# Optimization experiments

Measured on AMD Instinct MI355X. Metric: run time of the kernel, lower is better.

## Reference

```python
import jax, jax.numpy as jnp
import numpy as np
import math

B, LQ, LK = 2, 2048, 2048
DIM = 1024
H = 16
DH = DIM // H


def setup_inputs() -> dict:
    key = jax.random.key(0)
    ks = jax.random.split(key, 12)
    s = 1.0 / math.sqrt(DIM)
    return {
        "query": jax.random.normal(ks[0], (B, LQ, DIM), jnp.float32),
        "key": jax.random.normal(ks[1], (B, LK, DIM), jnp.float32),
        "value": jax.random.normal(ks[2], (B, LK, DIM), jnp.float32),
        "mask": jnp.zeros((B, LQ, LK), dtype=bool),
        "Wq": jax.random.normal(ks[3], (DIM, DIM), jnp.float32) * s,
        "bq": jax.random.normal(ks[4], (DIM,), jnp.float32) * s,
        "Wk": jax.random.normal(ks[5], (DIM, DIM), jnp.float32) * s,
        "bk": jax.random.normal(ks[6], (DIM,), jnp.float32) * s,
        "Wv": jax.random.normal(ks[7], (DIM, DIM), jnp.float32) * s,
        "bv": jax.random.normal(ks[8], (DIM,), jnp.float32) * s,
        "Wo": jax.random.normal(ks[9], (DIM, DIM), jnp.float32) * s,
        "bo": jax.random.normal(ks[10], (DIM,), jnp.float32) * s,
    }


def reference(query, key, value, mask, Wq, bq, Wk, bk, Wv, bv, Wo, bo):
    b = query.shape[0]

    def shape(x):  # (b, l, dim) -> (b, h, l, dh)
        return x.reshape(b, -1, H, DH).transpose(0, 2, 1, 3)

    q = shape(query @ Wq.T + bq)
    k = shape(key @ Wk.T + bk)
    v = shape(value @ Wv.T + bv)

    q = q / math.sqrt(DH)
    # (b, h, lq, lk) score matrix, computed in float32 as the original does
    scores = jnp.einsum("bhqd,bhkd->bhqk", q, k).astype(jnp.float32)
    scores = jnp.where(mask[:, None, :, :], jnp.float32(-1e18), scores)
    attn = jax.nn.softmax(scores, axis=-1).astype(q.dtype)
    context = jnp.einsum("bhqk,bhkd->bhqd", attn, v)
    context = context.transpose(0, 2, 1, 3).reshape(b, -1, H * DH)
    return context @ Wo.T + bo
```

## Files before the change

### kernel.cpp

```cpp
#include <hip/hip_runtime.h>
#include <hip/hip_bf16.h>

typedef __attribute__((ext_vector_type(4))) float float4v;
typedef __attribute__((ext_vector_type(8))) __bf16 bf16x8;
typedef __attribute__((ext_vector_type(4))) unsigned short ushort4v;
typedef __attribute__((ext_vector_type(8))) unsigned short ushort8v;

#define MFMA16(a, b, c) __builtin_amdgcn_mfma_f32_16x16x32_bf16(a, b, c, 0, 0, 0)

__device__ __forceinline__ unsigned short f2bf(float f) {
    return __builtin_bit_cast(unsigned short, (__bf16)f);
}

__device__ __forceinline__ float fast_exp2(float x) {
#if __has_builtin(__builtin_amdgcn_exp2f)
    return __builtin_amdgcn_exp2f(x);
#else
    return exp2f(x);
#endif
}

__device__ __forceinline__ void gl_lds16(const unsigned short* g, unsigned short* l) {
    __builtin_amdgcn_global_load_lds(
        (const __attribute__((address_space(1))) void*)g,
        (__attribute__((address_space(3))) void*)l, 16, 0, 0);
}

struct CvtSeg { const float* s; unsigned short* d; int n; };
struct Cvt4 { CvtSeg seg[4]; };

__global__ __launch_bounds__(256) void cvt_kernel(Cvt4 a) {
    const CvtSeg c = a.seg[blockIdx.y];
    const int stride = gridDim.x * 256 * 8;
    for (int i = (blockIdx.x * 256 + threadIdx.x) * 8; i < c.n; i += stride) {
        float4v v0 = *(const float4v*)(c.s + i);
        float4v v1 = *(const float4v*)(c.s + i + 4);
        ushort8v u;
        u[0] = f2bf(v0.x); u[1] = f2bf(v0.y); u[2] = f2bf(v0.z); u[3] = f2bf(v0.w);
        u[4] = f2bf(v1.x); u[5] = f2bf(v1.y); u[6] = f2bf(v1.z); u[7] = f2bf(v1.w);
        *(ushort8v*)(c.d + i) = u;
    }
}

__global__ __launch_bounds__(256) void gemm_qkv_kernel(
    const float* qa, const float* ka, const float* va,
    const unsigned short* Wqb, const unsigned short* Wkb, const unsigned short* Wvb,
    const float* bq, const float* bk, const float* bv,
    unsigned short* Qb, unsigned short* Kb, unsigned short* Vb, float qscale) {
    __shared__ unsigned short As[128 * 64];
    __shared__ unsigned short Ws[128 * 64];
    const int id = blockIdx.x;
    const int work = (id & 7) * 96 + (id >> 3);
    const int x = work & 31;
    const int combo = work >> 5;
    const int y = combo & 7;
    const int z = combo >> 3;
    const float* A = z == 0 ? qa : (z == 1 ? ka : va);
    const unsigned short* W = z == 0 ? Wqb : (z == 1 ? Wkb : Wvb);
    const float* bias = z == 0 ? bq : (z == 1 ? bk : bv);
    unsigned short* Cout = z == 0 ? Qb : (z == 1 ? Kb : Vb);
    const float scale = z == 0 ? qscale : 1.0f;
    const int m0 = x * 128, n0 = y * 128;
    const int N = 1024, K = 1024;

    const int t = threadIdx.x;
    const int w = t >> 6, lane = t & 63;
    const int quad = lane >> 4, l16 = lane & 15;
    const int wm = (w >> 1) * 64, wn = (w & 1) * 64;

    float4v acc[4][4];
    for (int i = 0; i < 4; ++i)
        for (int j = 0; j < 4; ++j) acc[i][j] = float4v{0.f, 0.f, 0.f, 0.f};

    const int srow = lane >> 3;
    const int scol = (lane & 7) * 8;

    for (int k0 = 0; k0 < K; k0 += 64) {
        float4v fa[4][2];
        for (int i = 0; i < 4; ++i) {
            const int c = w * 4 + i;
            const float* src = A + (size_t)(m0 + c * 8 + srow) * K + k0 + scol;
            fa[i][0] = *(const float4v*)src;
            fa[i][1] = *(const float4v*)(src + 4);
        }
        __syncthreads();
        for (int i = 0; i < 4; ++i) {
            const int c = w * 4 + i;
            ushort8v u;
            u[0] = f2bf(fa[i][0].x); u[1] = f2bf(fa[i][0].y);
            u[2] = f2bf(fa[i][0].z); u[3] = f2bf(fa[i][0].w);
            u[4] = f2bf(fa[i][1].x); u[5] = f2bf(fa[i][1].y);
            u[6] = f2bf(fa[i][1].z); u[7] = f2bf(fa[i][1].w);
            *(ushort8v*)&As[c * 512 + lane * 8] = u;
            gl_lds16(W + (size_t)(n0 + c * 8 + srow) * K + k0 + scol,
                     &Ws[c * 512 + lane * 8]);
        }
        __syncthreads();
        for (int ks = 0; ks < 2; ++ks) {
            bf16x8 af[4], wf[4];
            for (int i = 0; i < 4; ++i)
                af[i] = *(const bf16x8*)&As[(wm + i * 16 + l16) * 64 + ks * 32 + quad * 8];
            for (int i = 0; i < 4; ++i)
                wf[i] = *(const bf16x8*)&Ws[(wn + i * 16 + l16) * 64 + ks * 32 + quad * 8];
            for (int mi = 0; mi < 4; ++mi)
                for (int ni = 0; ni < 4; ++ni)
                    acc[mi][ni] = MFMA16(af[mi], wf[ni], acc[mi][ni]);
        }
    }

    for (int mi = 0; mi < 4; ++mi)
        for (int ni = 0; ni < 4; ++ni) {
            const int col = n0 + wn + ni * 16 + l16;
            const float bv = bias[col];
            for (int reg = 0; reg < 4; ++reg) {
                const int row = m0 + wm + mi * 16 + quad * 4 + reg;
                Cout[(size_t)row * N + col] = f2bf((acc[mi][ni][reg] + bv) * scale);
            }
        }
}

__global__ __launch_bounds__(256) void gemm_out_kernel(const unsigned short* __restrict__ A,
                                                       const unsigned short* __restrict__ W,
                                                       const float* __restrict__ bias,
                                                       float* __restrict__ Cout) {
    __shared__ unsigned short As[64 * 64];
    __shared__ unsigned short Ws[128 * 64];
    const int N = 1024, K = 1024;
    const int t = threadIdx.x;
    const int w = t >> 6, lane = t & 63;
    const int quad = lane >> 4, l16 = lane & 15;
    const int m0 = blockIdx.x * 64, n0 = blockIdx.y * 128;
    const int wm = (w & 1) * 32, wn = (w >> 1) * 64;

    float4v acc[2][4];
    for (int i = 0; i < 2; ++i)
        for (int j = 0; j < 4; ++j) acc[i][j] = float4v{0.f, 0.f, 0.f, 0.f};

    const int srow = lane >> 3;
    const int scol = (lane & 7) * 8;

    for (int k0 = 0; k0 < K; k0 += 64) {
        __syncthreads();
        for (int i = 0; i < 2; ++i) {
            const int c = w * 2 + i;
            gl_lds16(A + (size_t)(m0 + c * 8 + srow) * K + k0 + scol,
                     &As[c * 512 + lane * 8]);
        }
        for (int i = 0; i < 4; ++i) {
            const int c = w * 4 + i;
            gl_lds16(W + (size_t)(n0 + c * 8 + srow) * K + k0 + scol,
                     &Ws[c * 512 + lane * 8]);
        }
        __syncthreads();
        for (int ks = 0; ks < 2; ++ks) {
            bf16x8 af[2], wf[4];
            for (int i = 0; i < 2; ++i)
                af[i] = *(const bf16x8*)&As[(wm + i * 16 + l16) * 64 + ks * 32 + quad * 8];
            for (int i = 0; i < 4; ++i)
                wf[i] = *(const bf16x8*)&Ws[(wn + i * 16 + l16) * 64 + ks * 32 + quad * 8];
            for (int mi = 0; mi < 2; ++mi)
                for (int ni = 0; ni < 4; ++ni)
                    acc[mi][ni] = MFMA16(af[mi], wf[ni], acc[mi][ni]);
        }
    }

    for (int mi = 0; mi < 2; ++mi)
        for (int ni = 0; ni < 4; ++ni) {
            const int col = n0 + wn + ni * 16 + l16;
            const float bv = bias[col];
            for (int reg = 0; reg < 4; ++reg) {
                const int row = m0 + wm + mi * 16 + quad * 4 + reg;
                Cout[(size_t)row * N + col] = acc[mi][ni][reg] + bv;
            }
        }
}

__global__ __launch_bounds__(256) void attn_kernel(const unsigned short* __restrict__ Q,
                                                   const unsigned short* __restrict__ Kg,
                                                   const unsigned short* __restrict__ Vg,
                                                   const unsigned char* __restrict__ mask,
                                                   unsigned short* __restrict__ Ctx) {
    const int bid = blockIdx.x;
    const int bh = bid & 31;
    const int qt = bid >> 5;
    const int b = bh >> 4, h = bh & 15;
    const int t = threadIdx.x, w = t >> 6, lane = t & 63;
    const int quad = lane >> 4, l16 = lane & 15;

    __shared__ unsigned short Pt[128][72];
    __shared__ unsigned short Ks[64][72];
    __shared__ unsigned short Vt[64][72];

    const unsigned short* Qp = Q + ((size_t)(b * 2048 + qt * 128)) * 1024 + h * 64;
    const unsigned short* Kp = Kg + ((size_t)b * 2048) * 1024 + h * 64;
    const unsigned short* Vp = Vg + ((size_t)b * 2048) * 1024 + h * 64;
    const unsigned char* Mp = mask + (size_t)(b * 2048 + qt * 128) * 2048;

    for (int p = 0; p < 4; ++p) {
        const int idx = t + p * 256;
        const int r = idx >> 3, c8 = (idx & 7) * 8;
        *(uint4*)&Pt[r][c8] = *(const uint4*)(Qp + (size_t)r * 1024 + c8);
    }
    __syncthreads();
    bf16x8 qf[2][2];
    for (int c = 0; c < 2; ++c)
        for (int ks = 0; ks < 2; ++ks)
            qf[c][ks] = *(const bf16x8*)&Pt[w * 32 + c * 16 + l16][ks * 32 + quad * 8];

    float4v o[2][4];
    for (int c = 0; c < 2; ++c)
        for (int i = 0; i < 4; ++i) o[c][i] = float4v{0.f, 0.f, 0.f, 0.f};
    float l_acc[2] = {0.f, 0.f};

    const int sr = t >> 3, sc8 = (t & 7) * 8;
    const int vkk = (t & 31) * 2, vd0 = (t >> 5) * 8;
    const int mrow = w * 32 + (lane >> 1);
    const int mc0 = (lane & 1) * 32;

    uint4 kreg0, kreg1, vreg0, vreg1, mreg0, mreg1;
    {
        kreg0 = *(const uint4*)(Kp + (size_t)sr * 1024 + sc8);
        kreg1 = *(const uint4*)(Kp + (size_t)(sr + 32) * 1024 + sc8);
        vreg0 = *(const uint4*)(Vp + (size_t)vkk * 1024 + vd0);
        vreg1 = *(const uint4*)(Vp + (size_t)(vkk + 1) * 1024 + vd0);
        mreg0 = *(const uint4*)(Mp + (size_t)mrow * 2048 + mc0);
        mreg1 = *(const uint4*)(Mp + (size_t)mrow * 2048 + mc0 + 16);
    }

    for (int kc = 0; kc < 2048; kc += 64) {
        __syncthreads();
        *(uint4*)&Ks[sr][sc8] = kreg0;
        *(uint4*)&Ks[sr + 32][sc8] = kreg1;
        {
            const unsigned short* pa = (const unsigned short*)&vreg0;
            const unsigned short* pb = (const unsigned short*)&vreg1;
            for (int j = 0; j < 8; ++j)
                *(unsigned int*)&Vt[vd0 + j][vkk] =
                    (unsigned int)pa[j] | ((unsigned int)pb[j] << 16);
        }
        const unsigned int mor = mreg0.x | mreg0.y | mreg0.z | mreg0.w |
                                 mreg1.x | mreg1.y | mreg1.z | mreg1.w;
        const bool anymask = __any(mor != 0);
        __syncthreads();

        const int kn = kc + 64;
        if (kn < 2048) {
            kreg0 = *(const uint4*)(Kp + (size_t)(kn + sr) * 1024 + sc8);
            kreg1 = *(const uint4*)(Kp + (size_t)(kn + sr + 32) * 1024 + sc8);
            vreg0 = *(const uint4*)(Vp + (size_t)(kn + vkk) * 1024 + vd0);
            vreg1 = *(const uint4*)(Vp + (size_t)(kn + vkk + 1) * 1024 + vd0);
            mreg0 = *(const uint4*)(Mp + (size_t)mrow * 2048 + kn + mc0);
            mreg1 = *(const uint4*)(Mp + (size_t)mrow * 2048 + kn + mc0 + 16);
        }

        float4v s0[4], s1[4];
        for (int nt = 0; nt < 4; ++nt) {
            const float4v z4 = float4v{0.f, 0.f, 0.f, 0.f};
            bf16x8 kf = *(const bf16x8*)&Ks[nt * 16 + l16][quad * 8];
            s0[nt] = MFMA16(kf, qf[0][0], z4);
            s1[nt] = MFMA16(kf, qf[1][0], z4);
            kf = *(const bf16x8*)&Ks[nt * 16 + l16][32 + quad * 8];
            s0[nt] = MFMA16(kf, qf[0][1], s0[nt]);
            s1[nt] = MFMA16(kf, qf[1][1], s1[nt]);
        }

        for (int ks = 0; ks < 2; ++ks) {
            for (int c = 0; c < 2; ++c) {
                float4v* s = c ? s1 : s0;
                const int qrow = w * 32 + c * 16 + l16;
                float lc = l_acc[c];
                for (int nt = ks * 2; nt < ks * 2 + 2; ++nt) {
                    float p0 = s[nt][0], p1 = s[nt][1], p2 = s[nt][2], p3 = s[nt][3];
                    if (anymask) {
                        const unsigned char* mr =
                            Mp + (size_t)qrow * 2048 + kc + nt * 16 + quad * 4;
                        if (mr[0]) p0 = -1e18f;
                        if (mr[1]) p1 = -1e18f;
                        if (mr[2]) p2 = -1e18f;
                        if (mr[3]) p3 = -1e18f;
                    }
                    const float e0 = fast_exp2(p0), e1 = fast_exp2(p1);
                    const float e2 = fast_exp2(p2), e3 = fast_exp2(p3);
                    lc += (e0 + e1) + (e2 + e3);
                    uint2 u;
                    u.x = (unsigned int)f2bf(e0) | ((unsigned int)f2bf(e1) << 16);
                    u.y = (unsigned int)f2bf(e2) | ((unsigned int)f2bf(e3) << 16);
                    *(uint2*)&Pt[qrow][nt * 16 + quad * 4] = u;
                }
                l_acc[c] = lc;
            }
            bf16x8 pf0 = *(const bf16x8*)&Pt[w * 32 + l16][ks * 32 + quad * 8];
            bf16x8 pf1 = *(const bf16x8*)&Pt[w * 32 + 16 + l16][ks * 32 + quad * 8];
            for (int dt = 0; dt < 4; ++dt) {
                bf16x8 vf = *(const bf16x8*)&Vt[dt * 16 + l16][ks * 32 + quad * 8];
                o[0][dt] = MFMA16(pf0, vf, o[0][dt]);
                o[1][dt] = MFMA16(pf1, vf, o[1][dt]);
            }
        }
    }

    float lfull[2];
    for (int c = 0; c < 2; ++c) {
        float l = l_acc[c];
        l += __shfl_xor(l, 16);
        l += __shfl_xor(l, 32);
        lfull[c] = l;
    }

    for (int c = 0; c < 2; ++c) {
        float inv[4];
        for (int reg = 0; reg < 4; ++reg)
            inv[reg] = 1.0f / __shfl(lfull[c], (lane & 48) | (quad * 4 + reg));
        for (int dt = 0; dt < 4; ++dt) {
            const int dcol = dt * 16 + l16;
            for (int reg = 0; reg < 4; ++reg) {
                const int ql = w * 32 + c * 16 + quad * 4 + reg;
                Ctx[((size_t)(b * 2048 + qt * 128 + ql)) * 1024 + h * 64 + dcol] =
                    f2bf(o[c][dt][reg] * inv[reg]);
            }
        }
    }
}

extern "C" void kernel_launch(void* const* d_in, const int* in_sizes, int n_in,
                              void* d_out, int out_size, void* d_ws, size_t ws_size,
                              hipStream_t stream) {
    (void)in_sizes; (void)n_in; (void)out_size; (void)ws_size;
    const float* query = (const float*)d_in[0];
    const float* key   = (const float*)d_in[1];
    const float* value = (const float*)d_in[2];
    const unsigned char* mask = (const unsigned char*)d_in[3];
    const float* Wq = (const float*)d_in[4];
    const float* bq = (const float*)d_in[5];
    const float* Wk = (const float*)d_in[6];
    const float* bk = (const float*)d_in[7];
    const float* Wv = (const float*)d_in[8];
    const float* bv = (const float*)d_in[9];
    const float* Wo = (const float*)d_in[10];
    const float* bo = (const float*)d_in[11];

    const size_t MD = (size_t)4096 * 1024;
    const size_t WD = (size_t)1024 * 1024;

    unsigned short* Qb  = (unsigned short*)d_ws;
    unsigned short* Kb  = Qb + MD;
    unsigned short* Vb  = Kb + MD;
    unsigned short* Wqb = Vb + MD;
    unsigned short* Wkb = Wqb + WD;
    unsigned short* Wvb = Wkb + WD;
    unsigned short* Wob = Wvb + WD;
    unsigned short* Cb  = Wob + WD;

    Cvt4 cv;
    cv.seg[0] = {Wq, Wqb, (int)WD};
    cv.seg[1] = {Wk, Wkb, (int)WD};
    cv.seg[2] = {Wv, Wvb, (int)WD};
    cv.seg[3] = {Wo, Wob, (int)WD};
    cvt_kernel<<<dim3(512, 4), 256, 0, stream>>>(cv);

    const float qscale = 0.125f * 1.44269504088896f;
    gemm_qkv_kernel<<<dim3(768), 256, 0, stream>>>(
        query, key, value, Wqb, Wkb, Wvb, bq, bk, bv, Qb, Kb, Vb, qscale);

    attn_kernel<<<dim3(512), 256, 0, stream>>>(Qb, Kb, Vb, mask, Cb);

    gemm_out_kernel<<<dim3(64, 8), 256, 0, stream>>>(Cb, Wob, bo, (float*)d_out);
}
```

Measured before the change: 275.3 us.

## Double-buffer LDS in QKV and output projection GEMMs to overlap loads with MFMA

```diff
diff --git a/kernel.cpp b/kernel.cpp
--- a/kernel.cpp
+++ b/kernel.cpp
@@ -25,6 +25,14 @@
         (const __attribute__((address_space(1))) void*)g,
         (__attribute__((address_space(3))) void*)l, 16, 0, 0);
 }
+
+__device__ __forceinline__ void bar_raw() {
+    __builtin_amdgcn_sched_barrier(0);
+    __builtin_amdgcn_s_barrier();
+    __builtin_amdgcn_sched_barrier(0);
+}
+
+__device__ __forceinline__ void sbar() { __builtin_amdgcn_sched_barrier(0); }
 
 struct CvtSeg { const float* s; unsigned short* d; int n; };
 struct Cvt4 { CvtSeg seg[4]; };
@@ -47,8 +55,8 @@
     const unsigned short* Wqb, const unsigned short* Wkb, const unsigned short* Wvb,
     const float* bq, const float* bk, const float* bv,
     unsigned short* Qb, unsigned short* Kb, unsigned short* Vb, float qscale) {
-    __shared__ unsigned short As[128 * 64];
-    __shared__ unsigned short Ws[128 * 64];
+    __shared__ unsigned short As[2][128 * 64];
+    __shared__ unsigned short Ws[2][128 * 64];
     const int id = blockIdx.x;
     const int work = (id & 7) * 96 + (id >> 3);
     const int x = work & 31;
@@ -75,38 +83,83 @@
     const int srow = lane >> 3;
     const int scol = (lane & 7) * 8;
 
-    for (int k0 = 0; k0 < K; k0 += 64) {
-        float4v fa[4][2];
-        for (int i = 0; i < 4; ++i) {
-            const int c = w * 4 + i;
-            const float* src = A + (size_t)(m0 + c * 8 + srow) * K + k0 + scol;
-            fa[i][0] = *(const float4v*)src;
-            fa[i][1] = *(const float4v*)(src + 4);
-        }
-        __syncthreads();
-        for (int i = 0; i < 4; ++i) {
-            const int c = w * 4 + i;
-            ushort8v u;
-            u[0] = f2bf(fa[i][0].x); u[1] = f2bf(fa[i][0].y);
-            u[2] = f2bf(fa[i][0].z); u[3] = f2bf(fa[i][0].w);
-            u[4] = f2bf(fa[i][1].x); u[5] = f2bf(fa[i][1].y);
-            u[6] = f2bf(fa[i][1].z); u[7] = f2bf(fa[i][1].w);
-            *(ushort8v*)&As[c * 512 + lane * 8] = u;
-            gl_lds16(W + (size_t)(n0 + c * 8 + srow) * K + k0 + scol,
-                     &Ws[c * 512 + lane * 8]);
-        }
-        __syncthreads();
-        for (int ks = 0; ks < 2; ++ks) {
-            bf16x8 af[4], wf[4];
-            for (int i = 0; i < 4; ++i)
-                af[i] = *(const bf16x8*)&As[(wm + i * 16 + l16) * 64 + ks * 32 + quad * 8];
-            for (int i = 0; i < 4; ++i)
-                wf[i] = *(const bf16x8*)&Ws[(wn + i * 16 + l16) * 64 + ks * 32 + quad * 8];
-            for (int mi = 0; mi < 4; ++mi)
-                for (int ni = 0; ni < 4; ++ni)
-                    acc[mi][ni] = MFMA16(af[mi], wf[ni], acc[mi][ni]);
-        }
-    }
+    float4v faA[4][2], faB[4][2];
+
+#define LOAD_A(dst, tile)                                                     \
+    _Pragma("unroll") for (int i = 0; i < 4; ++i) {                           \
+        const int c = w * 4 + i;                                              \
+        const float* s_ = A + (size_t)(m0 + c * 8 + srow) * K + (tile) * 64 + scol; \
+        dst[i][0] = *(const float4v*)s_;                                      \
+        dst[i][1] = *(const float4v*)(s_ + 4);                                \
+    }
+#define STAGE_W(buf, tile)                                                    \
+    _Pragma("unroll") for (int i = 0; i < 4; ++i) {                           \
+        const int c = w * 4 + i;                                              \
+        gl_lds16(W + (size_t)(n0 + c * 8 + srow) * K + (tile) * 64 + scol,    \
+                 &Ws[buf][c * 512 + lane * 8]);                               \
+    }
+#define WRITE_A(buf, src)                                                     \
+    _Pragma("unroll") for (int i = 0; i < 4; ++i) {                           \
+        const int c = w * 4 + i;                                              \
+        ushort8v u;                                                           \
+        u[0] = f2bf(src[i][0].x); u[1] = f2bf(src[i][0].y);                   \
+        u[2] = f2bf(src[i][0].z); u[3] = f2bf(src[i][0].w);                   \
+        u[4] = f2bf(src[i][1].x); u[5] = f2bf(src[i][1].y);                   \
+        u[6] = f2bf(src[i][1].z); u[7] = f2bf(src[i][1].w);                   \
+        *(ushort8v*)&As[buf][c * 512 + lane * 8] = u;                         \
+    }
+#define MFMA_PHASE(buf)                                                       \
+    for (int ks = 0; ks < 2; ++ks) {                                          \
+        bf16x8 af[4], wf[4];                                                  \
+        for (int i = 0; i < 4; ++i)                                           \
+            af[i] = *(const bf16x8*)&As[buf][(wm + i * 16 + l16) * 64 + ks * 32 + quad * 8]; \
+        for (int i = 0; i < 4; ++i)                                           \
+            wf[i] = *(const bf16x8*)&Ws[buf][(wn + i * 16 + l16) * 64 + ks * 32 + quad * 8]; \
+        for (int mi = 0; mi < 4; ++mi)                                        \
+            for (int ni = 0; ni < 4; ++ni)                                    \
+                acc[mi][ni] = MFMA16(af[mi], wf[ni], acc[mi][ni]);            \
+    }
+
+    STAGE_W(0, 0);
+    sbar();
+    LOAD_A(faA, 0);
+    LOAD_A(faB, 1);
+    WRITE_A(0, faA);
+    sbar();
+    asm volatile("s_waitcnt vmcnt(8) lgkmcnt(0)" ::: "memory");
+    bar_raw();
+
+    for (int kk = 0; kk < 8; ++kk) {
+        const int te = kk * 2;
+        {
+            const int ta = (te + 2 < 16) ? te + 2 : 15;
+            STAGE_W(1, te + 1);
+            sbar();
+            LOAD_A(faA, ta);
+            WRITE_A(1, faB);
+            MFMA_PHASE(0);
+            sbar();
+            asm volatile("s_waitcnt vmcnt(8) lgkmcnt(0)" ::: "memory");
+            bar_raw();
+        }
+        {
+            const int to = te + 1;
+            const int tw = (to + 1 < 16) ? to + 1 : 15;
+            const int ta = (to + 2 < 16) ? to + 2 : 15;
+            STAGE_W(0, tw);
+            sbar();
+            LOAD_A(faB, ta);
+            WRITE_A(0, faA);
+            MFMA_PHASE(1);
+            sbar();
+            asm volatile("s_waitcnt vmcnt(8) lgkmcnt(0)" ::: "memory");
+            bar_raw();
+        }
+    }
+#undef LOAD_A
+#undef STAGE_W
+#undef WRITE_A
+#undef MFMA_PHASE
 
     for (int mi = 0; mi < 4; ++mi)
         for (int ni = 0; ni < 4; ++ni) {
@@ -123,8 +176,8 @@
                                                        const unsigned short* __restrict__ W,
                                                        const float* __restrict__ bias,
                                                        float* __restrict__ Cout) {
-    __shared__ unsigned short As[64 * 64];
-    __shared__ unsigned short Ws[128 * 64];
+    __shared__ unsigned short As[2][64 * 64];
+    __shared__ unsigned short Ws[2][128 * 64];
     const int N = 1024, K = 1024;
     const int t = threadIdx.x;
     const int w = t >> 6, lane = t & 63;
@@ -139,30 +192,54 @@
     const int srow = lane >> 3;
     const int scol = (lane & 7) * 8;
 
-    for (int k0 = 0; k0 < K; k0 += 64) {
-        __syncthreads();
-        for (int i = 0; i < 2; ++i) {
-            const int c = w * 2 + i;
-            gl_lds16(A + (size_t)(m0 + c * 8 + srow) * K + k0 + scol,
-                     &As[c * 512 + lane * 8]);
-        }
-        for (int i = 0; i < 4; ++i) {
-            const int c = w * 4 + i;
-            gl_lds16(W + (size_t)(n0 + c * 8 + srow) * K + k0 + scol,
-                     &Ws[c * 512 + lane * 8]);
-        }
-        __syncthreads();
-        for (int ks = 0; ks < 2; ++ks) {
-            bf16x8 af[2], wf[4];
-            for (int i = 0; i < 2; ++i)
-                af[i] = *(const bf16x8*)&As[(wm + i * 16 + l16) * 64 + ks * 32 + quad * 8];
-            for (int i = 0; i < 4; ++i)
-                wf[i] = *(const bf16x8*)&Ws[(wn + i * 16 + l16) * 64 + ks * 32 + quad * 8];
-            for (int mi = 0; mi < 2; ++mi)
-                for (int ni = 0; ni < 4; ++ni)
-                    acc[mi][ni] = MFMA16(af[mi], wf[ni], acc[mi][ni]);
-        }
-    }
+#define STAGE(buf, tile)                                                      \
+    _Pragma("unroll") for (int i = 0; i < 2; ++i) {                           \
+        const int c = w * 2 + i;                                              \
+        gl_lds16(A + (size_t)(m0 + c * 8 + srow) * K + (tile) * 64 + scol,    \
+                 &As[buf][c * 512 + lane * 8]);                               \
+    }                                                                         \
+    _Pragma("unroll") for (int i = 0; i < 4; ++i) {                           \
+        const int c = w * 4 + i;                                              \
+        gl_lds16(W + (size_t)(n0 + c * 8 + srow) * K + (tile) * 64 + scol,    \
+                 &Ws[buf][c * 512 + lane * 8]);                               \
+    }
+#define MFMA_PHASE(buf)                                                       \
+    for (int ks = 0; ks < 2; ++ks) {                                          \
+        bf16x8 af[2], wf[4];                                                  \
+        for (int i = 0; i < 2; ++i)                                           \
+            af[i] = *(const bf16x8*)&As[buf][(wm + i * 16 + l16) * 64 + ks * 32 + quad * 8]; \
+        for (int i = 0; i < 4; ++i)                                           \
+            wf[i] = *(const bf16x8*)&Ws[buf][(wn + i * 16 + l16) * 64 + ks * 32 + quad * 8]; \
+        for (int mi = 0; mi < 2; ++mi)                                        \
+            for (int ni = 0; ni < 4; ++ni)                                    \
+                acc[mi][ni] = MFMA16(af[mi], wf[ni], acc[mi][ni]);            \
+    }
+
+    STAGE(0, 0);
+    sbar();
+    asm volatile("s_waitcnt vmcnt(0)" ::: "memory");
+    bar_raw();
+
+    for (int kk = 0; kk < 8; ++kk) {
+        const int te = kk * 2;
+        {
+            STAGE(1, te + 1);
+            MFMA_PHASE(0);
+            sbar();
+            asm volatile("s_waitcnt vmcnt(0) lgkmcnt(0)" ::: "memory");
+            bar_raw();
+        }
+        {
+            const int tw = (te + 2 < 16) ? te + 2 : 15;
+            STAGE(0, tw);
+            MFMA_PHASE(1);
+            sbar();
+            asm volatile("s_waitcnt vmcnt(0) lgkmcnt(0)" ::: "memory");
+            bar_raw();
+        }
+    }
+#undef STAGE
+#undef MFMA_PHASE
 
     for (int mi = 0; mi < 2; ++mi)
         for (int ni = 0; ni < 4; ++ni) {
```

Measured after the change: 275.8 us. About the same (+0.2%).
